# Performance work log

Hardware: AMD Instinct MI355X
Metric: run time of the kernel (lower is better)

The kernel has to match this reference:

```python
import jax, jax.numpy as jnp
import numpy as np

N_NODES = 100000
N_EDGES = 1600000
IN_FEATS = 128
HEADS = 4
OUT_FEATS = 16
NEG_SLOPE = 0.2  # DGL GATConv default negative_slope


def setup_inputs() -> dict:
    key = jax.random.key(0)
    ks = jax.random.split(key, 7)
    feats = jax.random.normal(ks[0], (N_NODES, IN_FEATS), dtype=jnp.float32)
    W = jax.random.normal(ks[1], (HEADS * OUT_FEATS, IN_FEATS), dtype=jnp.float32) * 0.05
    attn_l = jax.random.normal(ks[2], (HEADS, OUT_FEATS), dtype=jnp.float32) * 0.1
    attn_r = jax.random.normal(ks[3], (HEADS, OUT_FEATS), dtype=jnp.float32) * 0.1
    bias = jax.random.normal(ks[4], (HEADS * OUT_FEATS,), dtype=jnp.float32) * 0.01
    src = jax.random.randint(ks[5], (N_EDGES,), 0, N_NODES, dtype=jnp.int64 if jax.config.jax_enable_x64 else jnp.int32)
    dst = jax.random.randint(ks[6], (N_EDGES,), 0, N_NODES, dtype=jnp.int64 if jax.config.jax_enable_x64 else jnp.int32)
    return {"feats": feats, "W": W, "attn_l": attn_l, "attn_r": attn_r,
            "bias": bias, "src": src, "dst": dst}


def reference(feats, W, attn_l, attn_r, bias, src, dst):
    """GATConv forward on a homogeneous graph built from concatenated edge lists.

    feats: [N, in_feats]; W: [H*F, in_feats]; attn_l/attn_r: [H, F]; bias: [H*F]
    src/dst: [E] edge endpoint indices. Returns [N, H, F] (DGL GATConv output).
    """
    N = feats.shape[0]
    H, F = attn_l.shape
    # Linear projection, per-head split: z [N, H, F]
    z = (feats @ W.T).reshape(N, H, F)
    # Per-node attention logits: el/er [N, H]
    el = jnp.einsum('nhf,hf->nh', z, attn_l)
    er = jnp.einsum('nhf,hf->nh', z, attn_r)
    # Per-edge unnormalized attention: e [E, H]
    e = jax.nn.leaky_relu(el[src] + er[dst], negative_slope=NEG_SLOPE)
    # Edge softmax over incoming edges of each destination node
    m = jax.ops.segment_max(e, dst, num_segments=N)           # [N, H]
    m = jnp.where(jnp.isfinite(m), m, jnp.zeros_like(m))      # guard empty segments
    ex = jnp.exp(e - m[dst])                                  # [E, H]
    denom = jax.ops.segment_sum(ex, dst, num_segments=N)      # [N, H]
    alpha = ex / denom[dst]                                   # [E, H]
    # Weighted message aggregation: scatter-add z[src] * alpha into dst
    msg = z[src] * alpha[:, :, None]                          # [E, H, F]
    out = jax.ops.segment_sum(msg, dst, num_segments=N)       # [N, H, F]
    return out + bias.reshape(1, H, F)
```

## Files before the change

kernel.cpp:

```cpp
#include <hip/hip_runtime.h>

#define N_NODES 100000
#define N_EDGES 1600000
#define IN_F    128
#define HEADS   4
#define OUT_F   16
#define HF      64
#define NEG_SLOPE 0.2f

#define BUCK    112
#define NBUCK   893
#define BSTRIDE 2048
#define BSC_CHUNK 6144
#define NB_BSC  261
#define BUCK3   56
#define K3_BLOCKS 1786
#define SCAP    1408

#define NB_MFMA2 391
#define NB_FUSED2 655

typedef __attribute__((ext_vector_type(8))) short short8;
typedef __attribute__((ext_vector_type(4))) float f32x4;

__device__ __forceinline__ short f2bf(float f) {
    union { float f; unsigned u; } v; v.f = f;
    return (short)((v.u + 0x7FFFu + ((v.u >> 16) & 1u)) >> 16);
}

__global__ __launch_bounds__(256) void k_prep(const float* __restrict__ W,
                                              const float* __restrict__ attn_l,
                                              const float* __restrict__ attn_r,
                                              unsigned short* __restrict__ Wfrag,
                                              int* __restrict__ gcur) {
    const int g = blockIdx.x, t = threadIdx.x;
    if (g >= 20) {
        int i = (g - 20) * 256 + t;
        if (i < 1024) gcur[i] = 0;
        return;
    }
    const int ct = g >> 2, kf = g & 3;
    #pragma unroll
    for (int e = 0; e < 2; ++e) {
        int off = e * 256 + t;
        int j = off & 7, lane = off >> 3;
        int n = lane & 15, qq = lane >> 4;
        int k = kf * 32 + qq * 8 + j;
        float v;
        if (ct < 4) {
            v = W[(size_t)(ct * 16 + n) * IN_F + k];
        } else if (n < 8) {
            int hh = n & 3;
            const float* at = (n < 4) ? attn_l : attn_r;
            v = 0.f;
            #pragma unroll
            for (int f = 0; f < 16; ++f)
                v += W[(size_t)(hh * 16 + f) * IN_F + k] * at[hh * 16 + f];
        } else {
            v = 0.f;
        }
        Wfrag[(size_t)g * 512 + off] = (unsigned short)f2bf(v);
    }
}

__global__ __launch_bounds__(1024) void k_fused(const float* __restrict__ feats,
                                                const unsigned short* __restrict__ Wfrag,
                                                unsigned short* __restrict__ zb,
                                                float* __restrict__ el,
                                                float* __restrict__ er,
                                                const int* __restrict__ src,
                                                const int* __restrict__ dst,
                                                int* __restrict__ gcur,
                                                unsigned* __restrict__ bin) {
    const unsigned bx = blockIdx.x;
    const unsigned q5 = bx / 5u, r5 = bx % 5u;
    const int t = threadIdx.x;

    if (r5 < 2u) {
        const int bid = (int)(q5 * 2u + r5);
        if (bid >= NB_BSC) return;
        __shared__ int h[NBUCK], cur[NBUCK];
        if (t < NBUCK) h[t] = 0;
        __syncthreads();
        const int start = bid * BSC_CHUNK;
        int end = start + BSC_CHUNK;
        if (end > N_EDGES) end = N_EDGES;

        int myd[6];
        #pragma unroll
        for (int k = 0; k < 6; ++k) {
            int i = start + t + k * 1024;
            myd[k] = (i < end) ? dst[i] : -1;
            if (myd[k] >= 0) atomicAdd(&h[(unsigned)myd[k] / BUCK], 1);
        }
        __syncthreads();
        if (t < NBUCK) cur[t] = h[t] ? atomicAdd(&gcur[t], h[t]) : 0;
        __syncthreads();
        #pragma unroll
        for (int k = 0; k < 6; ++k) {
            int i = start + t + k * 1024;
            if (i < end) {
                unsigned d = (unsigned)myd[k];
                unsigned b = d / BUCK;
                unsigned dl = d - b * BUCK;
                int pos = atomicAdd(&cur[b], 1);
                if (pos < BSTRIDE)
                    bin[(size_t)b * BSTRIDE + pos] = (unsigned)src[i] | (dl << 17);
            }
        }
        return;
    }

    const int bid = (int)(q5 * 3u + (r5 - 2u));
    if (bid >= NB_MFMA2) return;

    const int grp = t >> 6;
    const int l = t & 63;
    const int q = l >> 4, n = l & 15;

    short8 bfrag[5][4];
    #pragma unroll
    for (int ct = 0; ct < 5; ++ct)
        #pragma unroll
        for (int kf = 0; kf < 4; ++kf)
            bfrag[ct][kf] = *(const short8*)(Wfrag + (size_t)((ct * 4 + kf) * 64 + l) * 8);

    int anode = bid * 256 + grp * 16 + n;
    int aclamp = anode < N_NODES ? anode : 0;
    const float* arow = feats + (size_t)aclamp * IN_F + q * 8;

    f32x4 acc[5];
    #pragma unroll
    for (int ct = 0; ct < 5; ++ct) acc[ct] = (f32x4){0.f, 0.f, 0.f, 0.f};

    #pragma unroll
    for (int kf = 0; kf < 4; ++kf) {
        float4 x = *(const float4*)(arow + kf * 32);
        float4 y = *(const float4*)(arow + kf * 32 + 4);
        short8 a;
        a[0] = f2bf(x.x); a[1] = f2bf(x.y); a[2] = f2bf(x.z); a[3] = f2bf(x.w);
        a[4] = f2bf(y.x); a[5] = f2bf(y.y); a[6] = f2bf(y.z); a[7] = f2bf(y.w);
        #pragma unroll
        for (int ct = 0; ct < 5; ++ct)
            acc[ct] = __builtin_amdgcn_mfma_f32_16x16x32_bf16(a, bfrag[ct][kf], acc[ct], 0, 0, 0);
    }

    #pragma unroll
    for (int reg = 0; reg < 4; ++reg) {
        int onode = bid * 256 + grp * 16 + q * 4 + reg;
        if (onode >= N_NODES) continue;
        #pragma unroll
        for (int ct = 0; ct < 4; ++ct)
            zb[(size_t)onode * HF + ct * 16 + n] = (unsigned short)f2bf(acc[ct][reg]);
        float v4 = acc[4][reg];
        if (n < 4)       el[onode * HEADS + n] = v4;
        else if (n < 8)  er[onode * HEADS + (n - 4)] = v4;
    }
}

__global__ __launch_bounds__(256) void k3_sort(const unsigned* __restrict__ bin,
                                               const int* __restrict__ gcur,
                                               const float* __restrict__ el,
                                               const float* __restrict__ er,
                                               const unsigned short* __restrict__ zb,
                                               const float* __restrict__ bias,
                                               float* __restrict__ out) {
    __shared__ unsigned raw[BSTRIDE];
    __shared__ unsigned sorted[SCAP];
    __shared__ __align__(8) unsigned short exs[SCAP*4];
    __shared__ int hist[BUCK3];
    __shared__ int noff[BUCK3 + 1];
    __shared__ int cur[BUCK3];
    __shared__ int s[64];
    __shared__ float er_s[BUCK3 * HEADS];

    const int t = threadIdx.x;
    const int B2 = blockIdx.x >> 1;
    const int half = blockIdx.x & 1;
    const int dlo = half * BUCK3;
    const int nodebase = B2 * BUCK + dlo;
    const unsigned* mybin = bin + (size_t)B2 * BSTRIDE;
    int cnt = gcur[B2];
    if (cnt > BSTRIDE) cnt = BSTRIDE;

    if (t < BUCK3) hist[t] = 0;
    if (t < BUCK3 * HEADS) {
        int g = nodebase * HEADS + t;
        er_s[t] = (g < N_NODES * HEADS) ? er[g] : 0.f;
    }
    for (int i = t; i < cnt; i += 256) raw[i] = mybin[i];
    __syncthreads();

    for (int i = t; i < cnt; i += 256) {
        int d2 = (int)(raw[i] >> 17) - dlo;
        if ((unsigned)d2 < BUCK3) atomicAdd(&hist[d2], 1);
    }
    __syncthreads();

    if (t < 64) s[t] = (t < BUCK3) ? hist[t] : 0;
    __syncthreads();
    for (int o = 1; o < 64; o <<= 1) {
        int x = (t < 64 && t >= o) ? s[t - o] : 0;
        __syncthreads();
        if (t < 64) s[t] += x;
        __syncthreads();
    }
    if (t < BUCK3) {
        int excl = s[t] - hist[t];
        noff[t] = excl;
        cur[t] = excl;
    }
    if (t == 0) noff[BUCK3] = s[BUCK3 - 1];
    __syncthreads();

    for (int i = t; i < cnt; i += 256) {
        unsigned p = raw[i];
        int d2 = (int)(p >> 17) - dlo;
        if ((unsigned)d2 < BUCK3) {
            int pos = atomicAdd(&cur[d2], 1);
            if (pos < SCAP) {
                int sN = (int)(p & 0x1FFFF);
                float4 e4 = *(const float4*)(el + (size_t)sN * HEADS);
                float x0 = e4.x + er_s[d2 * HEADS + 0];
                float x1 = e4.y + er_s[d2 * HEADS + 1];
                float x2 = e4.z + er_s[d2 * HEADS + 2];
                float x3 = e4.w + er_s[d2 * HEADS + 3];
                x0 = x0 > 0.f ? x0 : NEG_SLOPE * x0;
                x1 = x1 > 0.f ? x1 : NEG_SLOPE * x1;
                x2 = x2 > 0.f ? x2 : NEG_SLOPE * x2;
                x3 = x3 > 0.f ? x3 : NEG_SLOPE * x3;
                unsigned short q0 = __builtin_bit_cast(unsigned short, (_Float16)__expf(x0));
                unsigned short q1 = __builtin_bit_cast(unsigned short, (_Float16)__expf(x1));
                unsigned short q2 = __builtin_bit_cast(unsigned short, (_Float16)__expf(x2));
                unsigned short q3 = __builtin_bit_cast(unsigned short, (_Float16)__expf(x3));
                sorted[pos] = (unsigned)sN;
                *(uint2*)(exs + pos * 4) =
                    make_uint2((unsigned)q0 | ((unsigned)q1 << 16),
                               (unsigned)q2 | ((unsigned)q3 << 16));
            }
        }
    }
    __syncthreads();

    const int wave = t >> 6, lane = t & 63;
    const int j = lane >> 3;
    const int c = lane & 7;
    const int h = c >> 1;

    for (int nl = wave; nl < BUCK3; nl += 4) {
        int node = nodebase + nl;
        if (node >= N_NODES) break;
        int nlo = noff[nl], nhi = noff[nl + 1];
        if (nhi > SCAP) nhi = SCAP;

        float4 A0 = make_float4(0.f, 0.f, 0.f, 0.f);
        float4 A1 = make_float4(0.f, 0.f, 0.f, 0.f);
        float den = 0.f;
        for (int i = nlo + j; i < nhi; i += 8) {
            int sN = (int)sorted[i];
            float ex = (float)__builtin_bit_cast(_Float16, exs[i * 4 + h]);
            uint4 v = *(const uint4*)(zb + (size_t)sN * HF + c * 8);
            den += ex;
            A0.x += ex * __uint_as_float(v.x << 16);
            A0.y += ex * __uint_as_float(v.x & 0xFFFF0000u);
            A0.z += ex * __uint_as_float(v.y << 16);
            A0.w += ex * __uint_as_float(v.y & 0xFFFF0000u);
            A1.x += ex * __uint_as_float(v.z << 16);
            A1.y += ex * __uint_as_float(v.z & 0xFFFF0000u);
            A1.z += ex * __uint_as_float(v.w << 16);
            A1.w += ex * __uint_as_float(v.w & 0xFFFF0000u);
        }
        #pragma unroll
        for (int m = 8; m <= 32; m <<= 1) {
            A0.x += __shfl_xor(A0.x, m); A0.y += __shfl_xor(A0.y, m);
            A0.z += __shfl_xor(A0.z, m); A0.w += __shfl_xor(A0.w, m);
            A1.x += __shfl_xor(A1.x, m); A1.y += __shfl_xor(A1.y, m);
            A1.z += __shfl_xor(A1.z, m); A1.w += __shfl_xor(A1.w, m);
            den  += __shfl_xor(den,  m);
        }
        if (j == 0) {
            float4 b0 = *(const float4*)(bias + c * 8);
            float4 b1 = *(const float4*)(bias + c * 8 + 4);
            if (den > 0.f) {
                float inv = 1.f / den;
                b0.x += A0.x * inv; b0.y += A0.y * inv;
                b0.z += A0.z * inv; b0.w += A0.w * inv;
                b1.x += A1.x * inv; b1.y += A1.y * inv;
                b1.z += A1.z * inv; b1.w += A1.w * inv;
            }
            *(float4*)(out + (size_t)node * HF + c * 8) = b0;
            *(float4*)(out + (size_t)node * HF + c * 8 + 4) = b1;
        }
    }
}

extern "C" void kernel_launch(void* const* d_in, const int* in_sizes, int n_in,
                              void* d_out, int out_size, void* d_ws, size_t ws_size,
                              hipStream_t stream) {
    const float* feats  = (const float*)d_in[0];
    const float* W      = (const float*)d_in[1];
    const float* attn_l = (const float*)d_in[2];
    const float* attn_r = (const float*)d_in[3];
    const float* bias   = (const float*)d_in[4];
    const int*   src    = (const int*)d_in[5];
    const int*   dst    = (const int*)d_in[6];
    float* out = (float*)d_out;

    char* ws = (char*)d_ws;
    unsigned short* zb = (unsigned short*)ws;  ws += (size_t)N_NODES * HF * 2;
    float* el    = (float*)ws;                 ws += N_NODES * HEADS * 4;
    float* er    = (float*)ws;                 ws += N_NODES * HEADS * 4;
    unsigned short* Wfrag = (unsigned short*)ws; ws += 20 * 64 * 8 * 2;
    int*   gcur  = (int*)ws;                   ws += 1024 * 4;
    unsigned* bin = (unsigned*)ws;             ws += (size_t)NBUCK * BSTRIDE * 4;

    k_prep  <<<24,         256,  0, stream>>>(W, attn_l, attn_r, Wfrag, gcur);
    k_fused <<<NB_FUSED2,  1024, 0, stream>>>(feats, Wfrag, zb, el, er, src, dst, gcur, bin);
    k3_sort <<<K3_BLOCKS,  256,  0, stream>>>(bin, gcur, el, er, zb, bias, out);
}
```

Baseline: 199.2 us.

## Process whole bucket per 512-thread block and recompute edge exp in aggregation

```diff
diff --git a/kernel.cpp b/kernel.cpp
--- a/kernel.cpp
+++ b/kernel.cpp
@@ -13,9 +13,6 @@
 #define BSTRIDE 2048
 #define BSC_CHUNK 6144
 #define NB_BSC  261
-#define BUCK3   56
-#define K3_BLOCKS 1786
-#define SCAP    1408
 
 #define NB_MFMA2 391
 #define NB_FUSED2 655
@@ -158,7 +155,7 @@
     }
 }
 
-__global__ __launch_bounds__(256) void k3_sort(const unsigned* __restrict__ bin,
+__global__ __launch_bounds__(512) void k3_sort(const unsigned* __restrict__ bin,
                                                const int* __restrict__ gcur,
                                                const float* __restrict__ el,
                                                const float* __restrict__ er,
@@ -166,79 +163,52 @@
                                                const float* __restrict__ bias,
                                                float* __restrict__ out) {
     __shared__ unsigned raw[BSTRIDE];
-    __shared__ unsigned sorted[SCAP];
-    __shared__ __align__(8) unsigned short exs[SCAP*4];
-    __shared__ int hist[BUCK3];
-    __shared__ int noff[BUCK3 + 1];
-    __shared__ int cur[BUCK3];
-    __shared__ int s[64];
-    __shared__ float er_s[BUCK3 * HEADS];
+    __shared__ unsigned sorted[BSTRIDE];
+    __shared__ int hist[BUCK];
+    __shared__ int noff[BUCK + 1];
+    __shared__ int cur[BUCK];
+    __shared__ int s[128];
+    __shared__ float er_s[BUCK * HEADS];
 
     const int t = threadIdx.x;
-    const int B2 = blockIdx.x >> 1;
-    const int half = blockIdx.x & 1;
-    const int dlo = half * BUCK3;
-    const int nodebase = B2 * BUCK + dlo;
-    const unsigned* mybin = bin + (size_t)B2 * BSTRIDE;
-    int cnt = gcur[B2];
+    const int B = blockIdx.x;
+    const int nodebase = B * BUCK;
+    const unsigned* mybin = bin + (size_t)B * BSTRIDE;
+    int cnt = gcur[B];
     if (cnt > BSTRIDE) cnt = BSTRIDE;
 
-    if (t < BUCK3) hist[t] = 0;
-    if (t < BUCK3 * HEADS) {
+    if (t < BUCK) hist[t] = 0;
+    if (t < BUCK * HEADS) {
         int g = nodebase * HEADS + t;
         er_s[t] = (g < N_NODES * HEADS) ? er[g] : 0.f;
     }
-    for (int i = t; i < cnt; i += 256) raw[i] = mybin[i];
-    __syncthreads();
-
-    for (int i = t; i < cnt; i += 256) {
-        int d2 = (int)(raw[i] >> 17) - dlo;
-        if ((unsigned)d2 < BUCK3) atomicAdd(&hist[d2], 1);
-    }
-    __syncthreads();
-
-    if (t < 64) s[t] = (t < BUCK3) ? hist[t] : 0;
-    __syncthreads();
-    for (int o = 1; o < 64; o <<= 1) {
-        int x = (t < 64 && t >= o) ? s[t - o] : 0;
-        __syncthreads();
-        if (t < 64) s[t] += x;
-        __syncthreads();
-    }
-    if (t < BUCK3) {
+    for (int i = t; i < cnt; i += 512) raw[i] = mybin[i];
+    __syncthreads();
+
+    for (int i = t; i < cnt; i += 512)
+        atomicAdd(&hist[raw[i] >> 17], 1);
+    __syncthreads();
+
+    if (t < 128) s[t] = (t < BUCK) ? hist[t] : 0;
+    __syncthreads();
+    for (int o = 1; o < 128; o <<= 1) {
+        int x = (t < 128 && t >= o) ? s[t - o] : 0;
+        __syncthreads();
+        if (t < 128) s[t] += x;
+        __syncthreads();
+    }
+    if (t < BUCK) {
         int excl = s[t] - hist[t];
         noff[t] = excl;
         cur[t] = excl;
     }
-    if (t == 0) noff[BUCK3] = s[BUCK3 - 1];
-    __syncthreads();
-
-    for (int i = t; i < cnt; i += 256) {
+    if (t == 0) noff[BUCK] = s[BUCK - 1];
+    __syncthreads();
+
+    for (int i = t; i < cnt; i += 512) {
         unsigned p = raw[i];
-        int d2 = (int)(p >> 17) - dlo;
-        if ((unsigned)d2 < BUCK3) {
-            int pos = atomicAdd(&cur[d2], 1);
-            if (pos < SCAP) {
-                int sN = (int)(p & 0x1FFFF);
-                float4 e4 = *(const float4*)(el + (size_t)sN * HEADS);
-                float x0 = e4.x + er_s[d2 * HEADS + 0];
-                float x1 = e4.y + er_s[d2 * HEADS + 1];
-                float x2 = e4.z + er_s[d2 * HEADS + 2];
-                float x3 = e4.w + er_s[d2 * HEADS + 3];
-                x0 = x0 > 0.f ? x0 : NEG_SLOPE * x0;
-                x1 = x1 > 0.f ? x1 : NEG_SLOPE * x1;
-                x2 = x2 > 0.f ? x2 : NEG_SLOPE * x2;
-                x3 = x3 > 0.f ? x3 : NEG_SLOPE * x3;
-                unsigned short q0 = __builtin_bit_cast(unsigned short, (_Float16)__expf(x0));
-                unsigned short q1 = __builtin_bit_cast(unsigned short, (_Float16)__expf(x1));
-                unsigned short q2 = __builtin_bit_cast(unsigned short, (_Float16)__expf(x2));
-                unsigned short q3 = __builtin_bit_cast(unsigned short, (_Float16)__expf(x3));
-                sorted[pos] = (unsigned)sN;
-                *(uint2*)(exs + pos * 4) =
-                    make_uint2((unsigned)q0 | ((unsigned)q1 << 16),
-                               (unsigned)q2 | ((unsigned)q3 << 16));
-            }
-        }
+        int pos = atomicAdd(&cur[p >> 17], 1);
+        sorted[pos] = p & 0x1FFFF;
     }
     __syncthreads();
 
@@ -246,21 +216,25 @@
     const int j = lane >> 3;
     const int c = lane & 7;
     const int h = c >> 1;
-
-    for (int nl = wave; nl < BUCK3; nl += 4) {
-        int node = nodebase + nl;
-        if (node >= N_NODES) break;
-        int nlo = noff[nl], nhi = noff[nl + 1];
-        if (nhi > SCAP) nhi = SCAP;
+    const int jj = j & 3;
+    const int sel = j >> 2;
+
+    for (int p = wave; p < BUCK / 2; p += 8) {
+        const int nl = p * 2 + sel;
+        const int node = nodebase + nl;
+        const int nlo = noff[nl], nhi = noff[nl + 1];
+        const float er_d = er_s[nl * HEADS + h];
 
         float4 A0 = make_float4(0.f, 0.f, 0.f, 0.f);
         float4 A1 = make_float4(0.f, 0.f, 0.f, 0.f);
         float den = 0.f;
-        for (int i = nlo + j; i < nhi; i += 8) {
+        for (int i = nlo + jj; i < nhi; i += 4) {
             int sN = (int)sorted[i];
-            float ex = (float)__builtin_bit_cast(_Float16, exs[i * 4 + h]);
+            float x = el[sN * HEADS + h] + er_d;
+            x = x > 0.f ? x : NEG_SLOPE * x;
+            float ex = __expf(x);
+            den += ex;
             uint4 v = *(const uint4*)(zb + (size_t)sN * HF + c * 8);
-            den += ex;
             A0.x += ex * __uint_as_float(v.x << 16);
             A0.y += ex * __uint_as_float(v.x & 0xFFFF0000u);
             A0.z += ex * __uint_as_float(v.y << 16);
@@ -271,14 +245,14 @@
             A1.w += ex * __uint_as_float(v.w & 0xFFFF0000u);
         }
         #pragma unroll
-        for (int m = 8; m <= 32; m <<= 1) {
+        for (int m = 8; m <= 16; m <<= 1) {
             A0.x += __shfl_xor(A0.x, m); A0.y += __shfl_xor(A0.y, m);
             A0.z += __shfl_xor(A0.z, m); A0.w += __shfl_xor(A0.w, m);
             A1.x += __shfl_xor(A1.x, m); A1.y += __shfl_xor(A1.y, m);
             A1.z += __shfl_xor(A1.z, m); A1.w += __shfl_xor(A1.w, m);
             den  += __shfl_xor(den,  m);
         }
-        if (j == 0) {
+        if (jj == 0 && node < N_NODES) {
             float4 b0 = *(const float4*)(bias + c * 8);
             float4 b1 = *(const float4*)(bias + c * 8 + 4);
             if (den > 0.f) {
@@ -316,5 +290,5 @@
 
     k_prep  <<<24,         256,  0, stream>>>(W, attn_l, attn_r, Wfrag, gcur);
     k_fused <<<NB_FUSED2,  1024, 0, stream>>>(feats, Wfrag, zb, el, er, src, dst, gcur, bin);
-    k3_sort <<<K3_BLOCKS,  256,  0, stream>>>(bin, gcur, el, er, zb, bias, out);
-}
+    k3_sort <<<NBUCK,      512,  0, stream>>>(bin, gcur, el, er, zb, bias, out);
+}
```

After: 172.1 us. 1.16x faster.
